# Kernel tuning notes

Hardware: AMD Instinct MI355X
Metric: run time of the kernel (lower is better)

The kernel has to match this reference:

```python
import jax, jax.numpy as jnp
import numpy as np

DT = 0.001          # time step
P = 2               # geomloss p -> cost = ||x-y||^2 / 2, eps = blur**p
BLUR = 0.01
SCALING = 0.5       # eps annealing ratio per step is SCALING**P
SPARSE = 1          # sparse_sampling
N_STEPS = 24        # fixed annealing+refinement iteration count (jit-static)


def setup_inputs() -> dict:
    key = jax.random.key(0)
    k1, k2 = jax.random.split(key)
    B, S, NT, NR = 2, 4, 256, 64
    syn_data = jax.random.normal(k1, (B, S, NT, NR), jnp.float32)
    obs_data = jax.random.normal(k2, (B, S, NT, NR), jnp.float32)
    return {"syn_data": syn_data, "obs_data": obs_data}


def _softmin(eps, C, h):
    # h: [m] = log-weights + potential/eps ; C: [n, m]
    return -eps * jax.nn.logsumexp(h[None, :] - C / eps, axis=1)


def _pairwise_cost(a, b):
    # geomloss p=2 cost: squared euclidean distance / 2
    return 0.5 * jnp.sum((a[:, None, :] - b[None, :, :]) ** 2, axis=-1)


def _sinkhorn_divergence(x, y):
    # x, y: [n, 2] point clouds with uniform weights 1/n.
    # Debiased Sinkhorn divergence S = OT_eps(x,y) - 0.5 OT(x,x) - 0.5 OT(y,y)
    # computed via log-domain iterations with epsilon annealing from
    # diameter**p down to blur**p (ratio scaling**p), as in geomloss.
    n = x.shape[0]
    la = jnp.full((n,), -np.log(n), x.dtype)  # log uniform weights
    Cxy = _pairwise_cost(x, y)
    Cyx = Cxy.T
    Cxx = _pairwise_cost(x, x)
    Cyy = _pairwise_cost(y, y)

    xy = jnp.concatenate([x, y], axis=0)
    diameter = jnp.max(jnp.max(xy, axis=0) - jnp.min(xy, axis=0))
    eps0 = diameter ** P
    eps_min = jnp.asarray(BLUR ** P, x.dtype)
    ratio = SCALING ** P
    eps_list = jnp.maximum(eps0 * ratio ** jnp.arange(N_STEPS, dtype=x.dtype), eps_min)

    zeros = jnp.zeros((n,), x.dtype)

    def step(carry, eps):
        f, g, px, py = carry
        f_new = _softmin(eps, Cxy, la + g / eps)
        g_new = _softmin(eps, Cyx, la + f / eps)
        # symmetric (debiasing) potentials use damped fixed-point updates
        px_new = 0.5 * (px + _softmin(eps, Cxx, la + px / eps))
        py_new = 0.5 * (py + _softmin(eps, Cyy, la + py / eps))
        return (f_new, g_new, px_new, py_new), None

    (f, g, px, py), _ = jax.lax.scan(step, (zeros, zeros, zeros, zeros), eps_list)
    w = jnp.exp(la)  # uniform 1/n
    return jnp.sum(w * (f - px)) + jnp.sum(w * (g - py))


def reference(syn_data, obs_data):
    B, S, NT, NR = syn_data.shape
    # trace mask: drop receiver only if BOTH obs and syn traces are all-zero
    mask1 = jnp.sum(jnp.abs(obs_data), axis=2) == 0  # [B,S,NR]
    mask2 = jnp.sum(jnp.abs(syn_data), axis=2) == 0
    mask = ~(mask1 & mask2)

    t = jnp.arange(NT, dtype=syn_data.dtype)[::SPARSE] * DT  # [NTs]
    obs_tr = jnp.swapaxes(obs_data[:, :, ::SPARSE, :], 2, 3)  # [B,S,NR,NTs]
    syn_tr = jnp.swapaxes(syn_data[:, :, ::SPARSE, :], 2, 3)
    tb = jnp.broadcast_to(t, obs_tr.shape)
    obs_pts = jnp.stack([tb, obs_tr], axis=-1)  # [B,S,NR,NTs,2]
    syn_pts = jnp.stack([tb, syn_tr], axis=-1)

    nts = obs_pts.shape[3]
    flat_obs = obs_pts.reshape(B * S * NR, nts, 2)
    flat_syn = syn_pts.reshape(B * S * NR, nts, 2)
    div = jax.vmap(_sinkhorn_divergence)(flat_obs, flat_syn)  # [B*S*NR]
    div = div.reshape(B, S, NR)
    return jnp.sum(jnp.where(mask, div, jnp.zeros_like(div)), axis=(1, 2))  # [B]
```

## Files before the change

kernel.cpp:

```cpp
#include <hip/hip_runtime.h>


constexpr int   N       = 256;
constexpr int   NPROB   = 512;
constexpr int   NRDIM   = 64;
constexpr float DT_F    = 0.001f;
constexpr float EPS_MIN = 1e-4f;
constexpr int   NSTEPS  = 24;
constexpr float LOG2E   = 1.4426950408889634f;
constexpr float LN2     = 0.6931471805599453f;
constexpr int   NT      = 512;
constexpr int   NG      = N / 2;

typedef float v2f __attribute__((ext_vector_type(2)));

extern "C" __global__ void __launch_bounds__(NT, 4)
sinkhorn_div_kernel(const float* __restrict__ syn,
                    const float* __restrict__ obs,
                    float* __restrict__ divs)
{
    const int p    = blockIdx.x;
    const int r    = p & (NRDIM - 1);
    const int bs   = p >> 6;
    const int tid  = threadIdx.x;
    const int row  = tid & (N - 1);
    const int pair = tid >> 8;

    __shared__ float4 yaH[2][NG];
    __shared__ float4 xaH[2][NG];
    __shared__ float4 yaW[NG];
    __shared__ float4 xaW[NG];
    __shared__ float  redA[32];

    float* yaHF = (float*)yaH;
    float* xaHF = (float*)xaH;
    float* yaWF = (float*)yaW;
    float* xaWF = (float*)xaW;

    const size_t base = (size_t)bs * N * NRDIM + r;
    const float xi = obs[base + (size_t)row * NRDIM];
    const float yi = syn[base + (size_t)row * NRDIM];
    const float ti = (float)row * DT_F;

    const int wslot = ((row >> 1) << 2) | (row & 1);

    if (pair == 0) {
        yaWF[wslot]     = yi;
        yaWF[wslot + 2] = ti;
    } else {
        xaWF[wslot]     = xi;
        xaWF[wslot + 2] = ti;
    }

    float hi = fmaxf(xi, yi), lo = fminf(xi, yi);
    float ax = fabsf(xi),     ay = fabsf(yi);
    #pragma unroll
    for (int off = 32; off > 0; off >>= 1) {
        hi  = fmaxf(hi, __shfl_down(hi, off, 64));
        lo  = fminf(lo, __shfl_down(lo, off, 64));
        ax += __shfl_down(ax, off, 64);
        ay += __shfl_down(ay, off, 64);
    }
    const int wave = tid >> 6;
    if ((tid & 63) == 0) {
        redA[wave * 4 + 0] = hi;  redA[wave * 4 + 1] = lo;
        redA[wave * 4 + 2] = ax;  redA[wave * 4 + 3] = ay;
    }
    __syncthreads();
    float vmax = -3.4e38f, vmin = 3.4e38f, sax = 0.0f, say = 0.0f;
    #pragma unroll
    for (int w = 0; w < 8; ++w) {
        vmax = fmaxf(vmax, redA[w * 4 + 0]);
        vmin = fminf(vmin, redA[w * 4 + 1]);
        sax += redA[w * 4 + 2];
        say += redA[w * 4 + 3];
    }

    const float tspread  = 255.0f * DT_F;
    const float diameter = fmaxf(tspread, vmax - vmin);
    float eps_raw = diameter * diameter;

    const float selfx = 0.5f * (ti * ti + xi * xi);
    const float selfy = 0.5f * (ti * ti + yi * yi);
    const float la2   = -8.0f;

    const float self1 = (pair == 0) ? selfx : selfy;
    const float self2 = (pair == 0) ? selfy : selfx;
    const float cf1   = (pair == 0) ? xi : yi;
    const float cf2   = (pair == 0) ? yi : xi;

    float pot1 = 0.0f, pot2 = 0.0f;

#define EXP2(x) __builtin_amdgcn_exp2f(x)

#define GRP(Q, W, AB, AC) do { \
        const v2f hb_ = {Q.x, Q.y}; const v2f hc_ = {Q.z, Q.w}; \
        const v2f zz_ = {W.x, W.y}; const v2f tt_ = {W.z, W.w}; \
        AB = __builtin_elementwise_fma(zz_, c1v, \
                 __builtin_elementwise_fma(tt_, tii2, hb_)); \
        AC = __builtin_elementwise_fma(zz_, c2v, \
                 __builtin_elementwise_fma(tt_, tii2, hc_)); \
    } while (0)

    for (int step = 0; step < NSTEPS; ++step) {
        const float eps = fmaxf(eps_raw, EPS_MIN);
        const float inv = LOG2E / eps;
        const int   buf = step & 1;
        const int   bo  = buf * (NG * 4);

        const float h1 = fmaf(pot1 - self1, inv, la2);
        const float h2 = fmaf(pot2 - self2, inv, la2);
        if (pair == 0) {
            xaHF[bo + wslot]     = h1;
            yaHF[bo + wslot + 2] = h2;
        } else {
            yaHF[bo + wslot]     = h1;
            xaHF[bo + wslot + 2] = h2;
        }
        __syncthreads();

        const float tii = ti * inv;
        const v2f tii2 = {tii, tii};
        const v2f c1v  = {cf1 * inv, cf1 * inv};
        const v2f c2v  = {cf2 * inv, cf2 * inv};
        const float4* __restrict__ Hq = (pair == 0) ? &yaH[buf][0] : &xaH[buf][0];
        const float4* __restrict__ Wq = (pair == 0) ? &yaW[0]      : &xaW[0];

        float m0 = -1e9f, m1 = -1e9f, s0 = 0.0f, s1 = 0.0f;
        #pragma unroll 2
        for (int k = 0; k < NG; k += 4) {
            const float4 Q0 = Hq[k + 0];
            const float4 Q1 = Hq[k + 1];
            const float4 Q2 = Hq[k + 2];
            const float4 Q3 = Hq[k + 3];
            const float4 W0 = Wq[k + 0];
            const float4 W1 = Wq[k + 1];
            const float4 W2 = Wq[k + 2];
            const float4 W3 = Wq[k + 3];
            v2f ab0, ab1, ab2, ab3, ac0, ac1, ac2, ac3;
            GRP(Q0, W0, ab0, ac0);
            GRP(Q1, W1, ab1, ac1);
            GRP(Q2, W2, ab2, ac2);
            GRP(Q3, W3, ab3, ac3);
            const float bt0 = fmaxf(fmaxf(ab0.x, ab0.y), ab1.x);
            const float bt1 = fmaxf(fmaxf(ab1.y, ab2.x), ab2.y);
            const float bt2 = fmaxf(fmaxf(ab3.x, ab3.y), m0);
            const float M0  = ceilf(fmaxf(fmaxf(bt0, bt1), bt2));
            const float ct0 = fmaxf(fmaxf(ac0.x, ac0.y), ac1.x);
            const float ct1 = fmaxf(fmaxf(ac1.y, ac2.x), ac2.y);
            const float ct2 = fmaxf(fmaxf(ac3.x, ac3.y), m1);
            const float M1  = ceilf(fmaxf(fmaxf(ct0, ct1), ct2));
            const v2f M0v = {M0, M0};
            const v2f M1v = {M1, M1};
            const v2f ub0 = ab0 - M0v, ub1 = ab1 - M0v;
            const v2f ub2 = ab2 - M0v, ub3 = ab3 - M0v;
            const v2f uc0 = ac0 - M1v, uc1 = ac1 - M1v;
            const v2f uc2 = ac2 - M1v, uc3 = ac3 - M1v;
            v2f eb0, eb1, eb2, eb3, ec0, ec1, ec2, ec3;
            eb0.x = EXP2(ub0.x); eb0.y = EXP2(ub0.y);
            eb1.x = EXP2(ub1.x); eb1.y = EXP2(ub1.y);
            eb2.x = EXP2(ub2.x); eb2.y = EXP2(ub2.y);
            eb3.x = EXP2(ub3.x); eb3.y = EXP2(ub3.y);
            ec0.x = EXP2(uc0.x); ec0.y = EXP2(uc0.y);
            ec1.x = EXP2(uc1.x); ec1.y = EXP2(uc1.y);
            ec2.x = EXP2(uc2.x); ec2.y = EXP2(uc2.y);
            ec3.x = EXP2(uc3.x); ec3.y = EXP2(uc3.y);
            const v2f pb0 = eb0 + eb1, pb1 = eb2 + eb3;
            const v2f qb  = pb0 + pb1;
            const v2f pc0 = ec0 + ec1, pc1 = ec2 + ec3;
            const v2f qc  = pc0 + pc1;
            s0 = ldexpf(s0, (int)(m0 - M0)) + (qb.x + qb.y);  m0 = M0;
            s1 = ldexpf(s1, (int)(m1 - M1)) + (qc.x + qc.y);  m1 = M1;
        }

        const float el2 = eps * LN2;
        pot1 = self1 - el2 * (m0 + __builtin_amdgcn_logf(s0));
        pot2 = 0.5f * (pot2 + (self2 - el2 * (m1 + __builtin_amdgcn_logf(s1))));

        eps_raw *= 0.25f;
    }
#undef GRP
#undef EXP2

    float contrib = pot1 - pot2;
    #pragma unroll
    for (int off = 32; off > 0; off >>= 1)
        contrib += __shfl_down(contrib, off, 64);
    __syncthreads();
    if ((tid & 63) == 0) redA[wave] = contrib;
    __syncthreads();
    if (tid == 0) {
        float total = 0.0f;
        #pragma unroll
        for (int w = 0; w < 8; ++w) total += redA[w];
        total *= (1.0f / (float)N);
        const bool masked_out = (sax == 0.0f) && (say == 0.0f);
        divs[p] = masked_out ? 0.0f : total;
    }
}

extern "C" __global__ void __launch_bounds__(256)
reduce_out_kernel(const float* __restrict__ divs, float* __restrict__ out)
{
    const int b   = blockIdx.x;
    const int tid = threadIdx.x;
    __shared__ float red[4];
    float v = divs[b * 256 + tid];
    #pragma unroll
    for (int off = 32; off > 0; off >>= 1)
        v += __shfl_down(v, off, 64);
    if ((tid & 63) == 0) red[tid >> 6] = v;
    __syncthreads();
    if (tid == 0) out[b] = red[0] + red[1] + red[2] + red[3];
}

extern "C" void kernel_launch(void* const* d_in, const int* in_sizes, int n_in,
                              void* d_out, int out_size, void* d_ws, size_t ws_size,
                              hipStream_t stream) {
    const float* syn = (const float*)d_in[0];
    const float* obs = (const float*)d_in[1];
    float* divs = (float*)d_ws;

    sinkhorn_div_kernel<<<NPROB, NT, 0, stream>>>(syn, obs, divs);
    reduce_out_kernel<<<2, 256, 0, stream>>>(divs, (float*)d_out);
}
```

Measured before the change: 544.7 us.

## Split each row's logsumexp over two half-waves with 1024-thread blocks

Doubles the threads per block so that each row's column reduction is split between the two 32-lane halves of a wave, each covering half the columns. The partial max and sum are then merged with a cross-half shuffle. The goal is to shorten the serial per-thread loop over 256 columns and raise the number of waves in flight per problem. The cost is duplicated per-row bookkeeping, the extra shuffle merge, and tighter register limits from the launch bound of 1024 threads with 8 blocks.

Result: slower. 600.0 us (+10.2%).

```diff
diff --git a/kernel.cpp b/kernel.cpp
--- a/kernel.cpp
+++ b/kernel.cpp
@@ -9,12 +9,12 @@
 constexpr int   NSTEPS  = 24;
 constexpr float LOG2E   = 1.4426950408889634f;
 constexpr float LN2     = 0.6931471805599453f;
-constexpr int   NT      = 512;
+constexpr int   NT      = 1024;
 constexpr int   NG      = N / 2;
 
 typedef float v2f __attribute__((ext_vector_type(2)));
 
-extern "C" __global__ void __launch_bounds__(NT, 4)
+extern "C" __global__ void __launch_bounds__(NT, 8)
 sinkhorn_div_kernel(const float* __restrict__ syn,
                     const float* __restrict__ obs,
                     float* __restrict__ divs)
@@ -23,14 +23,17 @@
     const int r    = p & (NRDIM - 1);
     const int bs   = p >> 6;
     const int tid  = threadIdx.x;
-    const int row  = tid & (N - 1);
-    const int pair = tid >> 8;
+    const int lane = tid & 63;
+    const int wave = tid >> 6;
+    const int pair = tid >> 9;
+    const int half = lane >> 5;
+    const int row  = ((wave & 7) << 5) | (lane & 31);
 
     __shared__ float4 yaH[2][NG];
     __shared__ float4 xaH[2][NG];
     __shared__ float4 yaW[NG];
     __shared__ float4 xaW[NG];
-    __shared__ float  redA[32];
+    __shared__ float  redA[64];
 
     float* yaHF = (float*)yaH;
     float* xaHF = (float*)xaH;
@@ -44,12 +47,14 @@
 
     const int wslot = ((row >> 1) << 2) | (row & 1);
 
-    if (pair == 0) {
-        yaWF[wslot]     = yi;
-        yaWF[wslot + 2] = ti;
-    } else {
-        xaWF[wslot]     = xi;
-        xaWF[wslot + 2] = ti;
+    if (half == 0) {
+        if (pair == 0) {
+            yaWF[wslot]     = yi;
+            yaWF[wslot + 2] = ti;
+        } else {
+            xaWF[wslot]     = xi;
+            xaWF[wslot + 2] = ti;
+        }
     }
 
     float hi = fmaxf(xi, yi), lo = fminf(xi, yi);
@@ -61,7 +66,6 @@
         ax += __shfl_down(ax, off, 64);
         ay += __shfl_down(ay, off, 64);
     }
-    const int wave = tid >> 6;
     if ((tid & 63) == 0) {
         redA[wave * 4 + 0] = hi;  redA[wave * 4 + 1] = lo;
         redA[wave * 4 + 2] = ax;  redA[wave * 4 + 3] = ay;
@@ -69,7 +73,7 @@
     __syncthreads();
     float vmax = -3.4e38f, vmin = 3.4e38f, sax = 0.0f, say = 0.0f;
     #pragma unroll
-    for (int w = 0; w < 8; ++w) {
+    for (int w = 0; w < 16; ++w) {
         vmax = fmaxf(vmax, redA[w * 4 + 0]);
         vmin = fminf(vmin, redA[w * 4 + 1]);
         sax += redA[w * 4 + 2];
@@ -90,6 +94,8 @@
     const float cf2   = (pair == 0) ? yi : xi;
 
     float pot1 = 0.0f, pot2 = 0.0f;
+
+    const int ghalf = half << 6;
 
 #define EXP2(x) __builtin_amdgcn_exp2f(x)
 
@@ -108,14 +114,16 @@
         const int   buf = step & 1;
         const int   bo  = buf * (NG * 4);
 
-        const float h1 = fmaf(pot1 - self1, inv, la2);
-        const float h2 = fmaf(pot2 - self2, inv, la2);
-        if (pair == 0) {
-            xaHF[bo + wslot]     = h1;
-            yaHF[bo + wslot + 2] = h2;
-        } else {
-            yaHF[bo + wslot]     = h1;
-            xaHF[bo + wslot + 2] = h2;
+        if (half == 0) {
+            const float h1 = fmaf(pot1 - self1, inv, la2);
+            const float h2 = fmaf(pot2 - self2, inv, la2);
+            if (pair == 0) {
+                xaHF[bo + wslot]     = h1;
+                yaHF[bo + wslot + 2] = h2;
+            } else {
+                yaHF[bo + wslot]     = h1;
+                xaHF[bo + wslot + 2] = h2;
+            }
         }
         __syncthreads();
 
@@ -128,7 +136,8 @@
 
         float m0 = -1e9f, m1 = -1e9f, s0 = 0.0f, s1 = 0.0f;
         #pragma unroll 2
-        for (int k = 0; k < NG; k += 4) {
+        for (int cc = 0; cc < 64; cc += 4) {
+            const int k = ghalf + cc;
             const float4 Q0 = Hq[k + 0];
             const float4 Q1 = Hq[k + 1];
             const float4 Q2 = Hq[k + 2];
@@ -173,6 +182,27 @@
             s1 = ldexpf(s1, (int)(m1 - M1)) + (qc.x + qc.y);  m1 = M1;
         }
 
+        {
+            const float mo = __shfl_xor(m0, 32, 64);
+            const float so = __shfl_xor(s0, 32, 64);
+            const float ml = (half == 0) ? m0 : mo;
+            const float sl = (half == 0) ? s0 : so;
+            const float mh = (half == 0) ? mo : m0;
+            const float sh = (half == 0) ? so : s0;
+            m0 = fmaxf(ml, mh);
+            s0 = ldexpf(sl, (int)(ml - m0)) + ldexpf(sh, (int)(mh - m0));
+        }
+        {
+            const float mo = __shfl_xor(m1, 32, 64);
+            const float so = __shfl_xor(s1, 32, 64);
+            const float ml = (half == 0) ? m1 : mo;
+            const float sl = (half == 0) ? s1 : so;
+            const float mh = (half == 0) ? mo : m1;
+            const float sh = (half == 0) ? so : s1;
+            m1 = fmaxf(ml, mh);
+            s1 = ldexpf(sl, (int)(ml - m1)) + ldexpf(sh, (int)(mh - m1));
+        }
+
         const float el2 = eps * LN2;
         pot1 = self1 - el2 * (m0 + __builtin_amdgcn_logf(s0));
         pot2 = 0.5f * (pot2 + (self2 - el2 * (m1 + __builtin_amdgcn_logf(s1))));
@@ -182,7 +212,7 @@
 #undef GRP
 #undef EXP2
 
-    float contrib = pot1 - pot2;
+    float contrib = (half == 0) ? (pot1 - pot2) : 0.0f;
     #pragma unroll
     for (int off = 32; off > 0; off >>= 1)
         contrib += __shfl_down(contrib, off, 64);
@@ -192,7 +222,7 @@
     if (tid == 0) {
         float total = 0.0f;
         #pragma unroll
-        for (int w = 0; w < 8; ++w) total += redA[w];
+        for (int w = 0; w < 16; ++w) total += redA[w];
         total *= (1.0f / (float)N);
         const bool masked_out = (sax == 0.0f) && (say == 0.0f);
         divs[p] = masked_out ? 0.0f : total;
```
